# Kernel tuning notes

Measured on AMD Instinct MI355X. Metric: run time of the kernel, lower is better.

Reference implementation:

```python
import jax, jax.numpy as jnp
import numpy as np

N = 100_000      # target ('paper') nodes
E_RAND = 500_000 # random metapath edges (self-loops added on top)
C = 256          # channels
H = 8            # heads
D = C // H       # proj_dim = 32
SEM = 128        # semantic attention hidden
NEG_SLOPE = 0.2


def _edges(k):
    e = jax.random.randint(k, (2, E_RAND), 0, N, dtype=jnp.int32)
    loops = jnp.broadcast_to(jnp.arange(N, dtype=jnp.int32), (2, N))
    return jnp.concatenate([e, loops], axis=1)  # [2, E_RAND + N]


def setup_inputs() -> dict:
    key = jax.random.key(0)
    ks = jax.random.split(key, 9)
    return {
        "x": jax.random.normal(ks[0], (N, C), dtype=jnp.float32),
        "W": jax.random.normal(ks[1], (D, C), dtype=jnp.float32) * (1.0 / np.sqrt(C)),
        "att1": jax.random.normal(ks[2], (H, 2 * D), dtype=jnp.float32) * (1.0 / np.sqrt(2 * D)),
        "att2": jax.random.normal(ks[3], (H, 2 * D), dtype=jnp.float32) * (1.0 / np.sqrt(2 * D)),
        "fc_w": jax.random.normal(ks[4], (SEM, C), dtype=jnp.float32) * (1.0 / np.sqrt(C)),
        "fc_b": jnp.zeros((SEM,), dtype=jnp.float32),
        "q": jax.random.normal(ks[5], (SEM,), dtype=jnp.float32) * (1.0 / np.sqrt(SEM)),
        "ei1": _edges(ks[6]),
        "ei2": _edges(ks[7]),
    }


def _segment_softmax(e, dst, num_nodes):
    # numerically stable softmax over edges grouped by destination node
    m = jax.ops.segment_max(e, dst, num_segments=num_nodes)      # [N, H]
    ex = jnp.exp(e - m[dst])                                     # [E, H]
    s = jax.ops.segment_sum(ex, dst, num_segments=num_nodes)     # [N, H]
    return ex / s[dst]


def _gat_layer(h, ei, att):
    # h: [N, d] projected target features; ei: [2, E]; att: [H, 2d]
    src, dst = ei[0], ei[1]
    n, d = h.shape
    a_dst, a_src = att[:, :d], att[:, d:]   # cat order in torch: [h_i(dst), h_j(src)]
    # per-edge attention logits [E, H] without materializing [E, H, 2d]
    e = jax.nn.leaky_relu(h[dst] @ a_dst.T + h[src] @ a_src.T, NEG_SLOPE)
    alpha = _segment_softmax(e, dst, n)                          # [E, H]
    m = h[src][:, None, :] * alpha[:, :, None]                   # [E, H, d]
    out = jax.ops.segment_sum(m, dst, num_segments=n)            # [N, H, d]
    return jax.nn.elu(out).reshape(n, H * d)                     # [N, H*d]


def reference(x, W, att1, att2, fc_w, fc_b, q, ei1, ei2):
    # type-specific projection (bias-free Linear): [N, C] -> [N, d]
    h = x @ W.T
    Z1 = _gat_layer(h, ei1, att1)
    Z2 = _gat_layer(h, ei2, att2)
    # semantic attention across meta-paths
    def score(Z):
        return (jnp.tanh(Z @ fc_w.T + fc_b) @ q).mean()
    V = jax.nn.softmax(jnp.stack([score(Z1), score(Z2)]))        # [2]
    return V[0] * Z1 + V[1] * Z2                                 # [N, C]
```

## Files before the change

### kernel.cpp

```cpp
#include <hip/hip_runtime.h>
#include <math.h>

#define Nn 100000
#define Cc 256
#define Dd 32
#define Hh 8
#define SEMk 128
#define PAD 32
#define NEG 0.2f

typedef __attribute__((ext_vector_type(8))) short bf16x8;
typedef __attribute__((ext_vector_type(4))) short s16x4;
typedef __attribute__((ext_vector_type(4))) float f32x4;

__device__ __forceinline__ short f2bf(float f) {
    unsigned u = __float_as_uint(f);
    u = (u + 0x7FFF + ((u >> 16) & 1)) >> 16;
    return (short)u;
}

__global__ __launch_bounds__(256) void k_wtrans(const float* __restrict__ W,
                                                float* __restrict__ Wt) {
    int i = blockIdx.x * 256 + threadIdx.x;
    if (i < Dd * Cc) {
        int j = i >> 5, k = i & 31;
        Wt[i] = W[k * Cc + j];
    }
}

__global__ __launch_bounds__(256) void k_fcwb(const float* __restrict__ fcw,
                                              short* __restrict__ fcwb) {
    int i = blockIdx.x * 256 + threadIdx.x;
    if (i < SEMk * Cc) fcwb[i] = f2bf(fcw[i]);
}

__global__ __launch_bounds__(256) void k_hproj(const float* __restrict__ x,
                                               const float* __restrict__ Wt,
                                               const float* __restrict__ att1,
                                               const float* __restrict__ att2,
                                               float* __restrict__ h,
                                               float* __restrict__ sd1, float* __restrict__ ss1,
                                               float* __restrict__ sd2, float* __restrict__ ss2) {
    __shared__ float4 xs[32 * 65];
    __shared__ float  wt[256 * 36];
    __shared__ float4 hs[32 * 9];
    __shared__ float  a1[8 * 68];
    __shared__ float  a2[8 * 68];

    int t = threadIdx.x;
    int nb = blockIdx.x * 32;

    const float4* xg = (const float4*)x + (size_t)nb * 64;
#pragma unroll
    for (int it = 0; it < 8; ++it) {
        int i = t + it * 256;
        xs[(i >> 6) * 65 + (i & 63)] = xg[i];
    }
    const float4* wg = (const float4*)Wt;
#pragma unroll
    for (int it = 0; it < 8; ++it) {
        int i = t + it * 256;
        *(float4*)&wt[(i >> 3) * 36 + (i & 7) * 4] = wg[i];
    }
#pragma unroll
    for (int it = 0; it < 2; ++it) {
        int i = t + it * 256;
        a1[(i >> 6) * 68 + (i & 63)] = att1[i];
        a2[(i >> 6) * 68 + (i & 63)] = att2[i];
    }
    __syncthreads();

    int nl = t >> 3;
    int dq = t & 7;
    float4 acc = make_float4(0.f, 0.f, 0.f, 0.f);
    const float4* xr = &xs[nl * 65];
#pragma unroll 4
    for (int j4 = 0; j4 < 64; ++j4) {
        float4 xv = xr[j4];
        float4 w0 = *(const float4*)&wt[(j4 * 4 + 0) * 36 + dq * 4];
        float4 w1 = *(const float4*)&wt[(j4 * 4 + 1) * 36 + dq * 4];
        float4 w2 = *(const float4*)&wt[(j4 * 4 + 2) * 36 + dq * 4];
        float4 w3 = *(const float4*)&wt[(j4 * 4 + 3) * 36 + dq * 4];
        acc.x += xv.x * w0.x + xv.y * w1.x + xv.z * w2.x + xv.w * w3.x;
        acc.y += xv.x * w0.y + xv.y * w1.y + xv.z * w2.y + xv.w * w3.y;
        acc.z += xv.x * w0.z + xv.y * w1.z + xv.z * w2.z + xv.w * w3.z;
        acc.w += xv.x * w0.w + xv.y * w1.w + xv.z * w2.w + xv.w * w3.w;
    }
    ((float4*)h)[(size_t)(nb + nl) * 8 + dq] = acc;
    hs[nl * 9 + dq] = acc;
    __syncthreads();

    int nl2 = t >> 3;
    int hh = t & 7;
    float d1 = 0.f, s1 = 0.f, d2 = 0.f, s2 = 0.f;
#pragma unroll
    for (int d4 = 0; d4 < 8; ++d4) {
        float4 hv = hs[nl2 * 9 + d4];
        float4 ad1 = *(const float4*)&a1[hh * 68 + d4 * 4];
        float4 as1 = *(const float4*)&a1[hh * 68 + 32 + d4 * 4];
        float4 ad2 = *(const float4*)&a2[hh * 68 + d4 * 4];
        float4 as2 = *(const float4*)&a2[hh * 68 + 32 + d4 * 4];
        d1 += hv.x * ad1.x + hv.y * ad1.y + hv.z * ad1.z + hv.w * ad1.w;
        s1 += hv.x * as1.x + hv.y * as1.y + hv.z * as1.z + hv.w * as1.w;
        d2 += hv.x * ad2.x + hv.y * ad2.y + hv.z * ad2.z + hv.w * ad2.w;
        s2 += hv.x * as2.x + hv.y * as2.y + hv.z * as2.z + hv.w * as2.w;
    }
    int n = nb + nl2;
    sd1[n * 8 + hh] = d1; ss1[n * 8 + hh] = s1;
    sd2[n * 8 + hh] = d2; ss2[n * 8 + hh] = s2;
}

__global__ __launch_bounds__(256) void k_scatter(const int* __restrict__ ei, int E,
                                                 int* __restrict__ cnt, int* __restrict__ slots) {
    int e = blockIdx.x * 256 + threadIdx.x;
    if (e >= E) return;
    int s = ei[e];
    int d = ei[E + e];
    int pos = atomicAdd(&cnt[d], 1);
    if (pos < PAD) slots[d * PAD + pos] = s;
}

__global__ __launch_bounds__(256) void k_gat(const float* __restrict__ h,
                                             const float* __restrict__ sdst,
                                             const float* __restrict__ ssrc,
                                             const int* __restrict__ cnt,
                                             const int* __restrict__ slots,
                                             float* __restrict__ Z) {
    int gid = blockIdx.x * 256 + threadIdx.x;
    int n = gid >> 6;
    int lane = gid & 63;
    if (n >= Nn) return;
    int deg = cnt[n]; if (deg > PAD) deg = PAD;
    int hh = lane >> 3;
    int sub = lane & 7;
    float sd = sdst[n * 8 + hh];
    int sval = slots[n * PAD + (lane & 31)];

    float ssum = 0.f;
    float4 acc = make_float4(0.f, 0.f, 0.f, 0.f);
    const float4* h4 = (const float4*)h;
#pragma unroll 2
    for (int i = 0; i < deg; ++i) {
        int s = __shfl(sval, i);
        float ev = sd + ssrc[s * 8 + hh];
        ev = ev > 0.f ? ev : NEG * ev;
        float w = __expf(ev);
        float4 hv = h4[(size_t)s * 8 + sub];
        acc.x += w * hv.x; acc.y += w * hv.y; acc.z += w * hv.z; acc.w += w * hv.w;
        ssum += w;
    }
    float inv = 1.f / ssum;
    float4 o;
    o.x = acc.x * inv; o.y = acc.y * inv; o.z = acc.z * inv; o.w = acc.w * inv;
    o.x = o.x > 0.f ? o.x : __expf(o.x) - 1.f;
    o.y = o.y > 0.f ? o.y : __expf(o.y) - 1.f;
    o.z = o.z > 0.f ? o.z : __expf(o.z) - 1.f;
    o.w = o.w > 0.f ? o.w : __expf(o.w) - 1.f;
    ((float4*)Z)[(size_t)n * 64 + lane] = o;
}

__device__ __forceinline__ float fast_tanh(float x) {
    return 1.f - 2.f / (1.f + __expf(2.f * x));
}

__global__ void k_score(const float* __restrict__ Z,
                        const short* __restrict__ fcwb,
                        const float* __restrict__ fcb,
                        const float* __restrict__ q,
                        float* __restrict__ Sacc) {
    __shared__ short zs[64 * 264];
    __shared__ float partial[4];
    int t = threadIdx.x;

    const float4* Zg4 = (const float4*)Z + (size_t)blockIdx.x * 4096;
    size_t gmax = (size_t)Nn * 64 - (size_t)blockIdx.x * 4096;
#pragma unroll
    for (int it = 0; it < 16; ++it) {
        int idx = it * 256 + t;
        if ((size_t)idx < gmax) {
            float4 v = Zg4[idx];
            int row = idx >> 6, c4 = idx & 63;
            s16x4 b;
            b[0] = f2bf(v.x); b[1] = f2bf(v.y); b[2] = f2bf(v.z); b[3] = f2bf(v.w);
            *(s16x4*)&zs[row * 264 + c4 * 4] = b;
        }
    }
    __syncthreads();

    int lane = t & 63;
    int wid = t >> 6;
    int nodebase = blockIdx.x * 64 + wid * 16;
    float local = 0.f;
    if (nodebase < Nn) {
        int col = lane & 15;
        int quad = lane >> 4;

        f32x4 acc[8];
#pragma unroll
        for (int tt = 0; tt < 8; ++tt) { acc[tt][0] = 0.f; acc[tt][1] = 0.f; acc[tt][2] = 0.f; acc[tt][3] = 0.f; }

        const short* zrow = &zs[(wid * 16 + col) * 264 + quad * 8];
        const short* brow = fcwb + (size_t)col * Cc + quad * 8;
#pragma unroll
        for (int ks = 0; ks < 8; ++ks) {
            bf16x8 a = *(const bf16x8*)(zrow + ks * 32);
            bf16x8 bf[8];
#pragma unroll
            for (int tt = 0; tt < 8; ++tt)
                bf[tt] = *(const bf16x8*)(brow + tt * 4096 + ks * 32);
#pragma unroll
            for (int tt = 0; tt < 8; ++tt)
                acc[tt] = __builtin_amdgcn_mfma_f32_16x16x32_bf16(a, bf[tt], acc[tt], 0, 0, 0);
        }

#pragma unroll
        for (int tt = 0; tt < 8; ++tt) {
            int n = tt * 16 + col;
            float b = fcb[n], qq = q[n];
#pragma unroll
            for (int r = 0; r < 4; ++r) local += fast_tanh(acc[tt][r] + b) * qq;
        }
    }
#pragma unroll
    for (int off = 32; off > 0; off >>= 1) local += __shfl_down(local, off);
    if (lane == 0) partial[wid] = local;
    __syncthreads();
    if (t == 0) {
        float s = partial[0] + partial[1] + partial[2] + partial[3];
        atomicAdd(&Sacc[blockIdx.x & 15], s);
    }
}

__global__ __launch_bounds__(256) void k_combine(float* __restrict__ out,
                                                 const float* __restrict__ Z2,
                                                 const float* __restrict__ S) {
    float s1 = 0.f, s2 = 0.f;
#pragma unroll
    for (int i = 0; i < 16; ++i) { s1 += S[i]; s2 += S[16 + i]; }
    s1 *= (1.f / (float)Nn);
    s2 *= (1.f / (float)Nn);
    float mx = fmaxf(s1, s2);
    float e1 = __expf(s1 - mx), e2 = __expf(s2 - mx);
    float inv = 1.f / (e1 + e2);
    float V0 = e1 * inv, V1 = e2 * inv;
    size_t i = (size_t)blockIdx.x * 256 + threadIdx.x;
    if (i < (size_t)Nn * 64) {
        float4 a = ((float4*)out)[i];
        float4 b = ((const float4*)Z2)[i];
        a.x = V0 * a.x + V1 * b.x;
        a.y = V0 * a.y + V1 * b.y;
        a.z = V0 * a.z + V1 * b.z;
        a.w = V0 * a.w + V1 * b.w;
        ((float4*)out)[i] = a;
    }
}

extern "C" void kernel_launch(void* const* d_in, const int* in_sizes, int n_in,
                              void* d_out, int out_size, void* d_ws, size_t ws_size,
                              hipStream_t stream) {
    const float* x    = (const float*)d_in[0];
    const float* W    = (const float*)d_in[1];
    const float* att1 = (const float*)d_in[2];
    const float* att2 = (const float*)d_in[3];
    const float* fcw  = (const float*)d_in[4];
    const float* fcb  = (const float*)d_in[5];
    const float* q    = (const float*)d_in[6];
    const int*   ei1  = (const int*)d_in[7];
    const int*   ei2  = (const int*)d_in[8];
    int E1 = in_sizes[7] / 2;
    int E2 = in_sizes[8] / 2;
    float* out = (float*)d_out;

    char* ws = (char*)d_ws;
    size_t off = 0;
    auto alloc = [&](size_t bytes) -> char* {
        char* p = ws + off;
        off = (off + bytes + 255) & ~(size_t)255;
        return p;
    };
    float* Z2   = (float*)alloc((size_t)Nn * Cc * 4);
    float* h    = (float*)alloc((size_t)Nn * Dd * 4);
    float* sd1  = (float*)alloc((size_t)Nn * Hh * 4);
    float* ss1  = (float*)alloc((size_t)Nn * Hh * 4);
    float* sd2  = (float*)alloc((size_t)Nn * Hh * 4);
    float* ss2  = (float*)alloc((size_t)Nn * Hh * 4);
    int*   cnt  = (int*)alloc((size_t)2 * Nn * 4);
    float* red  = (float*)alloc(256);
    float* Wt   = (float*)alloc((size_t)Dd * Cc * 4);
    short* fcwb = (short*)alloc((size_t)SEMk * Cc * 2);
    int*   slt1 = (int*)alloc((size_t)Nn * PAD * 4);
    int*   slt2 = (int*)alloc((size_t)Nn * PAD * 4);
    (void)ws_size; (void)n_in; (void)out_size;

    hipMemsetAsync(cnt, 0, (size_t)2 * Nn * 4, stream);
    hipMemsetAsync(red, 0, 256, stream);

    k_wtrans<<<(Dd * Cc + 255) / 256, 256, 0, stream>>>(W, Wt);
    k_fcwb<<<(SEMk * Cc + 255) / 256, 256, 0, stream>>>(fcw, fcwb);
    k_hproj<<<Nn / 32, 256, 0, stream>>>(x, Wt, att1, att2, h, sd1, ss1, sd2, ss2);
    k_scatter<<<(E1 + 255) / 256, 256, 0, stream>>>(ei1, E1, cnt, slt1);
    k_scatter<<<(E2 + 255) / 256, 256, 0, stream>>>(ei2, E2, cnt + Nn, slt2);
    k_gat<<<(Nn * 64) / 256, 256, 0, stream>>>(h, sd1, ss1, cnt, slt1, out);
    k_gat<<<(Nn * 64) / 256, 256, 0, stream>>>(h, sd2, ss2, cnt + Nn, slt2, Z2);
    int nblk = (Nn + 63) / 64;
    k_score<<<nblk, 256, 0, stream>>>(out, fcwb, fcb, q, red);
    k_score<<<nblk, 256, 0, stream>>>(Z2, fcwb, fcb, q, red + 16);
    k_combine<<<(Nn * 64) / 256, 256, 0, stream>>>(out, Z2, red);
}
```

Before: 605.4 us.

## Fuse semantic score MFMA into GAT aggregation and batch neighbor gathers

Merges the semantic-attention scoring into the GAT aggregation kernel. Each 512-thread block handles 8 nodes, writes their bf16 outputs to LDS, and runs a 16x16x32 MFMA against fc_w, with each wave covering 16 semantic units. This removes the separate k_score launches and the re-read of Z from global memory. The neighbor loop is also restructured to issue 8 gathers at once, masking the tail to raise memory-level parallelism. In exchange, half of each MFMA tile is wasted on padding rows, and every block rereads all of fc_w.

```diff
diff --git a/kernel.cpp b/kernel.cpp
--- a/kernel.cpp
+++ b/kernel.cpp
@@ -120,34 +120,62 @@
     if (pos < PAD) slots[d * PAD + pos] = s;
 }
 
-__global__ __launch_bounds__(256) void k_gat(const float* __restrict__ h,
-                                             const float* __restrict__ sdst,
-                                             const float* __restrict__ ssrc,
-                                             const int* __restrict__ cnt,
-                                             const int* __restrict__ slots,
-                                             float* __restrict__ Z) {
-    int gid = blockIdx.x * 256 + threadIdx.x;
-    int n = gid >> 6;
-    int lane = gid & 63;
-    if (n >= Nn) return;
-    int deg = cnt[n]; if (deg > PAD) deg = PAD;
+__device__ __forceinline__ float fast_tanh(float x) {
+    return 1.f - 2.f / (1.f + __expf(2.f * x));
+}
+
+__global__ __launch_bounds__(512, 4) void k_gat(const float* __restrict__ h,
+                                                const float* __restrict__ sdst,
+                                                const float* __restrict__ ssrc,
+                                                const int* __restrict__ cnt,
+                                                const int* __restrict__ slots,
+                                                float* __restrict__ Z,
+                                                const short* __restrict__ fcwb,
+                                                const float* __restrict__ fcb,
+                                                const float* __restrict__ q,
+                                                float* __restrict__ Sacc, int bin) {
+    __shared__ short zls[16 * 264];
+    __shared__ float partial[8];
+    int t = threadIdx.x;
+    int lane = t & 63;
+    int wid = t >> 6;
+    int n = blockIdx.x * 8 + wid;
+
+    for (int i = t; i < 1056; i += 512) ((int*)&zls[8 * 264])[i] = 0;
+
     int hh = lane >> 3;
     int sub = lane & 7;
+    int deg = cnt[n]; if (deg > PAD) deg = PAD;
     float sd = sdst[n * 8 + hh];
     int sval = slots[n * PAD + (lane & 31)];
 
     float ssum = 0.f;
     float4 acc = make_float4(0.f, 0.f, 0.f, 0.f);
     const float4* h4 = (const float4*)h;
-#pragma unroll 2
-    for (int i = 0; i < deg; ++i) {
-        int s = __shfl(sval, i);
-        float ev = sd + ssrc[s * 8 + hh];
-        ev = ev > 0.f ? ev : NEG * ev;
-        float w = __expf(ev);
-        float4 hv = h4[(size_t)s * 8 + sub];
-        acc.x += w * hv.x; acc.y += w * hv.y; acc.z += w * hv.z; acc.w += w * hv.w;
-        ssum += w;
+    for (int base = 0; base < deg; base += 8) {
+        int s[8];
+        float ssv[8];
+        float4 hv[8];
+#pragma unroll
+        for (int i = 0; i < 8; ++i) {
+            int si = __shfl(sval, base + i);
+            s[i] = (base + i < deg) ? si : n;
+        }
+#pragma unroll
+        for (int i = 0; i < 8; ++i) {
+            ssv[i] = ssrc[(size_t)s[i] * 8 + hh];
+            hv[i]  = h4[(size_t)s[i] * 8 + sub];
+        }
+#pragma unroll
+        for (int i = 0; i < 8; ++i) {
+            float ev = sd + ssv[i];
+            ev = ev > 0.f ? ev : NEG * ev;
+            float w = __expf(ev);
+            w = (base + i < deg) ? w : 0.f;
+            acc.x += w * hv[i].x; acc.y += w * hv[i].y;
+            acc.z += w * hv[i].z; acc.w += w * hv[i].w;
+            ssum += w;
+        }
     }
     float inv = 1.f / ssum;
     float4 o;
@@ -157,77 +185,39 @@
     o.z = o.z > 0.f ? o.z : __expf(o.z) - 1.f;
     o.w = o.w > 0.f ? o.w : __expf(o.w) - 1.f;
     ((float4*)Z)[(size_t)n * 64 + lane] = o;
-}
-
-__device__ __forceinline__ float fast_tanh(float x) {
-    return 1.f - 2.f / (1.f + __expf(2.f * x));
-}
-
-__global__ void k_score(const float* __restrict__ Z,
-                        const short* __restrict__ fcwb,
-                        const float* __restrict__ fcb,
-                        const float* __restrict__ q,
-                        float* __restrict__ Sacc) {
-    __shared__ short zs[64 * 264];
-    __shared__ float partial[4];
-    int t = threadIdx.x;
-
-    const float4* Zg4 = (const float4*)Z + (size_t)blockIdx.x * 4096;
-    size_t gmax = (size_t)Nn * 64 - (size_t)blockIdx.x * 4096;
-#pragma unroll
-    for (int it = 0; it < 16; ++it) {
-        int idx = it * 256 + t;
-        if ((size_t)idx < gmax) {
-            float4 v = Zg4[idx];
-            int row = idx >> 6, c4 = idx & 63;
-            s16x4 b;
-            b[0] = f2bf(v.x); b[1] = f2bf(v.y); b[2] = f2bf(v.z); b[3] = f2bf(v.w);
-            *(s16x4*)&zs[row * 264 + c4 * 4] = b;
-        }
-    }
-    __syncthreads();
-
-    int lane = t & 63;
-    int wid = t >> 6;
-    int nodebase = blockIdx.x * 64 + wid * 16;
+
+    s16x4 b4;
+    b4[0] = f2bf(o.x); b4[1] = f2bf(o.y); b4[2] = f2bf(o.z); b4[3] = f2bf(o.w);
+    *(s16x4*)&zls[wid * 264 + lane * 4] = b4;
+    __syncthreads();
+
+    int col = lane & 15;
+    int quad = lane >> 4;
+    f32x4 sacc;
+    sacc[0] = 0.f; sacc[1] = 0.f; sacc[2] = 0.f; sacc[3] = 0.f;
+    const short* zrow = &zls[col * 264 + quad * 8];
+    const short* brow = fcwb + (size_t)(wid * 16 + col) * Cc + quad * 8;
+#pragma unroll
+    for (int ks = 0; ks < 8; ++ks) {
+        bf16x8 a = *(const bf16x8*)(zrow + ks * 32);
+        bf16x8 b = *(const bf16x8*)(brow + ks * 32);
+        sacc = __builtin_amdgcn_mfma_f32_16x16x32_bf16(a, b, sacc, 0, 0, 0);
+    }
     float local = 0.f;
-    if (nodebase < Nn) {
-        int col = lane & 15;
-        int quad = lane >> 4;
-
-        f32x4 acc[8];
-#pragma unroll
-        for (int tt = 0; tt < 8; ++tt) { acc[tt][0] = 0.f; acc[tt][1] = 0.f; acc[tt][2] = 0.f; acc[tt][3] = 0.f; }
-
-        const short* zrow = &zs[(wid * 16 + col) * 264 + quad * 8];
-        const short* brow = fcwb + (size_t)col * Cc + quad * 8;
-#pragma unroll
-        for (int ks = 0; ks < 8; ++ks) {
-            bf16x8 a = *(const bf16x8*)(zrow + ks * 32);
-            bf16x8 bf[8];
-#pragma unroll
-            for (int tt = 0; tt < 8; ++tt)
-                bf[tt] = *(const bf16x8*)(brow + tt * 4096 + ks * 32);
-#pragma unroll
-            for (int tt = 0; tt < 8; ++tt)
-                acc[tt] = __builtin_amdgcn_mfma_f32_16x16x32_bf16(a, bf[tt], acc[tt], 0, 0, 0);
-        }
-
-#pragma unroll
-        for (int tt = 0; tt < 8; ++tt) {
-            int n = tt * 16 + col;
-            float b = fcb[n], qq = q[n];
-#pragma unroll
-            for (int r = 0; r < 4; ++r) local += fast_tanh(acc[tt][r] + b) * qq;
-        }
+    if (quad < 2) {
+        int sem = wid * 16 + col;
+        float bb = fcb[sem], qq = q[sem];
+#pragma unroll
+        for (int r = 0; r < 4; ++r) local += fast_tanh(sacc[r] + bb) * qq;
     }
 #pragma unroll
     for (int off = 32; off > 0; off >>= 1) local += __shfl_down(local, off);
     if (lane == 0) partial[wid] = local;
     __syncthreads();
     if (t == 0) {
-        float s = partial[0] + partial[1] + partial[2] + partial[3];
-        atomicAdd(&Sacc[blockIdx.x & 15], s);
+        float s = partial[0] + partial[1] + partial[2] + partial[3]
+                + partial[4] + partial[5] + partial[6] + partial[7];
+        atomicAdd(&Sacc[bin + (blockIdx.x & 15)], s);
     }
 }
 
@@ -300,10 +290,7 @@
     k_hproj<<<Nn / 32, 256, 0, stream>>>(x, Wt, att1, att2, h, sd1, ss1, sd2, ss2);
     k_scatter<<<(E1 + 255) / 256, 256, 0, stream>>>(ei1, E1, cnt, slt1);
     k_scatter<<<(E2 + 255) / 256, 256, 0, stream>>>(ei2, E2, cnt + Nn, slt2);
-    k_gat<<<(Nn * 64) / 256, 256, 0, stream>>>(h, sd1, ss1, cnt, slt1, out);
-    k_gat<<<(Nn * 64) / 256, 256, 0, stream>>>(h, sd2, ss2, cnt + Nn, slt2, Z2);
-    int nblk = (Nn + 63) / 64;
-    k_score<<<nblk, 256, 0, stream>>>(out, fcwb, fcb, q, red);
-    k_score<<<nblk, 256, 0, stream>>>(Z2, fcwb, fcb, q, red + 16);
+    k_gat<<<Nn / 8, 512, 0, stream>>>(h, sd1, ss1, cnt, slt1, out, fcwb, fcb, q, red, 0);
+    k_gat<<<Nn / 8, 512, 0, stream>>>(h, sd2, ss2, cnt + Nn, slt2, Z2, fcwb, fcb, q, red, 16);
     k_combine<<<(Nn * 64) / 256, 256, 0, stream>>>(out, Z2, red);
 }
```

Measured after the change: 656.1 us. 1.08x slower.
